# Performance work log

Measured on AMD Instinct MI355X. Metric: run time of the kernel, lower is better.

The kernel has to match this reference:

```python
import jax, jax.numpy as jnp
import numpy as np
import math

ENC_MAX = 64
DEC_MAX = 128


def _tran_mask(M):
    # faithful reconstruction of self.tran and self.mask buffers
    fs = math.log(DEC_MAX / (DEC_MAX + ENC_MAX))  # fixed_shift_p
    fe = math.log(ENC_MAX / (DEC_MAX + ENC_MAX))  # fixed_emit_p
    i = np.arange(M)[:, None]
    j = np.arange(M)[None, :]
    tran = np.where(i + j < M, (M - (i + j) - 1) * fs + fe, 0.0).astype(np.float32)
    # mask_br: -inf where i+j >= M (anti-diagonal i+j==M-1 stays 0)
    mask = np.where(i + j >= M, -np.inf, 0.0).astype(np.float32)
    return jnp.asarray(tran), jnp.asarray(mask)


def _lstm(xs, Wih, Whh, bih, bhh):
    # xs: [L, in]; torch LSTM gate order i,f,g,o; batch=1 handled as unbatched
    H = Whh.shape[1]
    def step(carry, xt):
        h, c = carry
        g = Wih @ xt + bih + Whh @ h + bhh  # [4H]
        i, f, gg, o = jnp.split(g, 4)
        c = jax.nn.sigmoid(f) * c + jax.nn.sigmoid(i) * jnp.tanh(gg)
        h = jax.nn.sigmoid(o) * jnp.tanh(c)
        return (h, c), h
    _, hs = jax.lax.scan(step, (jnp.zeros((H,), xs.dtype), jnp.zeros((H,), xs.dtype)), xs)
    return hs  # [L, H]


def setup_inputs() -> dict:
    key = jax.random.key(0)
    ks = jax.random.split(key, 16)
    V, E, H, K, T = 32000, 100, 512, ENC_MAX, DEC_MAX
    def p(k, shape, scale):
        return jax.random.normal(k, shape, dtype=jnp.float32) * scale
    return {
        "x": jax.random.randint(ks[0], (1, K), 0, V),
        "y": jax.random.randint(ks[1], (1, T), 0, V),
        "emb": p(ks[2], (V, E), 0.1),
        "enc_Wih": p(ks[3], (4 * H, E), 1.0 / np.sqrt(E)),
        "enc_Whh": p(ks[4], (4 * H, H), 1.0 / np.sqrt(H)),
        "enc_bih": jnp.zeros((4 * H,), jnp.float32),
        "enc_bhh": jnp.zeros((4 * H,), jnp.float32),
        "dec_Wih": p(ks[5], (4 * H, E), 1.0 / np.sqrt(E)),
        "dec_Whh": p(ks[6], (4 * H, H), 1.0 / np.sqrt(H)),
        "dec_bih": jnp.zeros((4 * H,), jnp.float32),
        "dec_bhh": jnp.zeros((4 * H,), jnp.float32),
        "Weh": p(ks[7], (E, 2 * H), 1.0 / np.sqrt(2 * H)),  # emit_hidden
        "beh": jnp.zeros((E,), jnp.float32),
        "Wem": p(ks[8], (V, E), 1.0 / np.sqrt(E)),  # emit
        "bem": jnp.zeros((V,), jnp.float32),
    }


def reference(x, y, emb, enc_Wih, enc_Whh, enc_bih, enc_bhh,
              dec_Wih, dec_Whh, dec_bih, dec_bhh, Weh, beh, Wem, bem):
    K = x.shape[1]
    T = y.shape[1]
    x_emb = emb[x[0]]            # [K, E]
    y_emb = emb[y[0]]            # [T, E]
    Eenc = _lstm(x_emb, enc_Wih, enc_Whh, enc_bih, enc_bhh)  # [K, H]
    D = _lstm(y_emb, dec_Wih, dec_Whh, dec_bih, dec_bhh)     # [T, H]

    tran, mask = _tran_mask(ENC_MAX)
    tranm = tran[ENC_MAX - K:, :K] + mask[ENC_MAX - K:, :K]  # [K, K]

    # emissions for all steps at once (joint = cat(E, D_{t-1}) -> relu -> emit -> log_softmax -> gather word_t)
    H = Eenc.shape[1]
    We_E, We_D = Weh[:, :H], Weh[:, H:]
    hpre = jax.nn.relu(Eenc @ We_E.T + (D[:T - 1] @ We_D.T)[:, None, :] + beh)  # [T-1, K, E]
    logits = jnp.einsum('tke,ve->tkv', hpre, Wem) + bem                          # [T-1, K, V]
    words = y[0, 1:]                                                             # [T-1]
    gathered = jnp.take_along_axis(logits, words[:, None, None], axis=2)[..., 0]  # [T-1, K]
    emission = gathered - jax.scipy.special.logsumexp(logits, axis=2)             # [T-1, K]

    def step(pre_alpha, em_t):
        scores = pre_alpha[:, None] + tranm            # [K(i), K(j)]
        mx = jnp.max(scores, axis=0)                   # [K]
        ind = jnp.argmax(scores, axis=0).astype(jnp.int32)
        mx = jnp.flip(mx)                              # self.flip
        ind = jnp.flip(ind)
        new = mx + em_t
        return new, ind

    pre_alpha, inds = jax.lax.scan(step, jnp.zeros((K,), jnp.float32), emission)
    indices = jnp.concatenate([jnp.zeros((1, K), jnp.int32), inds], axis=0)  # [T, K]

    val = pre_alpha[K - 1]  # align_last

    def bstep(ind, idx_row):
        nind = idx_row[ind]
        return nind, nind
    _, alignments = jax.lax.scan(bstep, jnp.int32(K - 1), indices, reverse=True)  # [T]
    return alignments, val
```

## Files before the change

### kernel.cpp

```cpp
#include <hip/hip_runtime.h>


#define K_ENC 64
#define HID   512
#define EMB   100
#define VOC   32000
#define G4    2048

typedef __attribute__((ext_vector_type(8))) short  short8;
typedef __attribute__((ext_vector_type(4))) float  f32x4;
typedef __attribute__((ext_vector_type(4))) int    i32x4;
typedef unsigned long long u64;

#define LOG2E 1.4426950408889634f
#define LN2   0.6931471805599453f

__device__ __forceinline__ unsigned short f2bf(float f) {
  union { float f; unsigned u; } x; x.f = f;
  unsigned r = x.u + 0x7FFFu + ((x.u >> 16) & 1u);
  return (unsigned short)(r >> 16);
}

__device__ __forceinline__ float fast_sigmoid(float x) {
  return __builtin_amdgcn_rcpf(1.f + __builtin_amdgcn_exp2f(-LOG2E * x));
}
__device__ __forceinline__ float fast_tanh(float x) {
  return 1.f - 2.f * __builtin_amdgcn_rcpf(1.f + __builtin_amdgcn_exp2f(2.f * LOG2E * x));
}

#define OFF_PAD   0
#define OFF_HBUF  256
#define OFF_G0E   4352
#define OFF_G0D   135424
#define OFF_EENC  395520
#define OFF_D     428288
#define OFF_EWE   493312
#define OFF_DWD   499712
#define OFF_BEM   512412
#define OFF_SUM   544412
#define OFF_EM    552540
#define OFF_WEM   560668

__global__ void kZero(float* __restrict__ ws) {
  int gid = blockIdx.x * 256 + threadIdx.x;
  if (gid < 4352) ws[gid] = 0.f;
  else if (gid < 4352 + 127 * 64) ws[OFF_SUM + gid - 4352] = 0.f;
}

__global__ __launch_bounds__(256) void kG0(const int* __restrict__ x, const int* __restrict__ y,
                    const float* __restrict__ emb,
                    const float* __restrict__ eWih, const float* __restrict__ ebih,
                    const float* __restrict__ ebhh,
                    const float* __restrict__ dWih, const float* __restrict__ dbih,
                    const float* __restrict__ dbhh,
                    float* __restrict__ ws) {
  int gid = blockIdx.x * 256 + threadIdx.x;
  const int enc_total = K_ENC * G4;
  if (gid >= enc_total + 127 * G4) return;
  bool enc = gid < enc_total;
  int loc = enc ? gid : gid - enc_total;
  int t = loc >> 11, r = loc & (G4 - 1);
  int tok = enc ? x[t] : y[t];
  const float* Wr = (enc ? eWih : dWih) + r * EMB;
  const float* er = emb + tok * EMB;
  float s = 0.f;
  #pragma unroll 4
  for (int e = 0; e < EMB; ++e) s += er[e] * Wr[e];
  s += enc ? (ebih[r] + ebhh[r]) : (dbih[r] + dbhh[r]);
  ws[(enc ? OFF_G0E : OFF_G0D) + t * G4 + r] = s;
}

__global__ __launch_bounds__(256) void kWemPrep(const float* __restrict__ Wem,
                                               const float* __restrict__ bem,
                                               float* __restrict__ ws) {
  int gid = blockIdx.x * 256 + threadIdx.x;
  int vt = gid >> 11;
  int kb = (gid >> 9) & 3;
  int L  = (gid >> 3) & 63;
  int j  = gid & 7;
  int v = vt * 16 + (L & 15);
  int k = kb * 32 + ((L >> 4) << 3) + j;
  float val = (k < EMB) ? Wem[v * EMB + k] : 0.f;
  ((unsigned short*)(ws + OFF_WEM))[gid] = f2bf(val);
  if (gid < VOC) ws[OFF_BEM + gid] = bem[gid] * LOG2E;
}

#define STEP_GUARD 16384

__global__ __launch_bounds__(512, 2) void kLstm(const float* __restrict__ eWhh,
                                                const float* __restrict__ dWhh,
                                                float* __restrict__ ws) {
  const int grp = blockIdx.x >> 5;
  const int wg  = blockIdx.x & 31;
  const float* __restrict__ Whh = grp ? dWhh : eWhh;
  const float* __restrict__ G0  = ws + (grp ? OFF_G0D : OFF_G0E);
  float* hs = ws + (grp ? OFF_D : OFF_EENC);
  u64* hb = (u64*)(ws + OFF_HBUF) + grp * 1024;
  const int steps = grp ? 127 : K_ENC;
  const int tid = threadIdx.x;
  const int jl = tid >> 5, sub = tid & 31;
  const int j = wg * 16 + jl;
  __shared__ float h_lds[32 * 20];

  float cst = 0.f;
  for (int t = 0; t < steps; ++t) {
    float4 w4[16];
    #pragma unroll
    for (int g = 0; g < 4; ++g)
      #pragma unroll
      for (int q = 0; q < 4; ++q)
        w4[g * 4 + q] = *(const float4*)&Whh[(g * HID + j) * HID + sub * 16 + q * 4];
    float g0i = G0[t * G4 + j];
    float g0f = G0[t * G4 + HID + j];
    float g0g = G0[t * G4 + 2 * HID + j];
    float g0o = G0[t * G4 + 3 * HID + j];
    if (tid < 256) {
      const u64* src = hb + (t & 1) * 512 + tid * 2;
      i32x4 v;
      int guard = 0;
      for (;;) {
        asm volatile("global_load_dwordx4 %0, %1, off sc0 sc1\n\t"
                     "s_waitcnt vmcnt(0)"
                     : "=v"(v) : "v"(src) : "memory");
        if ((v[1] == t && v[3] == t) || ++guard >= STEP_GUARD) break;
        __builtin_amdgcn_s_sleep(1);
      }
      int k0 = tid * 2, k1 = k0 + 1;
      union { int u; float f; } c0, c1; c0.u = v[0]; c1.u = v[2];
      h_lds[(k0 >> 4) * 20 + (k0 & 15)] = c0.f;
      h_lds[(k1 >> 4) * 20 + (k1 & 15)] = c1.f;
    }
    __syncthreads();
    float h[16];
    #pragma unroll
    for (int kk = 0; kk < 16; ++kk) h[kk] = h_lds[sub * 20 + kk];
    float p0 = 0.f, p1 = 0.f, p2 = 0.f, p3 = 0.f;
    #pragma unroll
    for (int q = 0; q < 4; ++q) {
      p0 += w4[0+q].x*h[q*4+0] + w4[0+q].y*h[q*4+1] + w4[0+q].z*h[q*4+2] + w4[0+q].w*h[q*4+3];
      p1 += w4[4+q].x*h[q*4+0] + w4[4+q].y*h[q*4+1] + w4[4+q].z*h[q*4+2] + w4[4+q].w*h[q*4+3];
      p2 += w4[8+q].x*h[q*4+0] + w4[8+q].y*h[q*4+1] + w4[8+q].z*h[q*4+2] + w4[8+q].w*h[q*4+3];
      p3 += w4[12+q].x*h[q*4+0] + w4[12+q].y*h[q*4+1] + w4[12+q].z*h[q*4+2] + w4[12+q].w*h[q*4+3];
    }
    #pragma unroll
    for (int d = 1; d <= 16; d <<= 1) {
      p0 += __shfl_xor(p0, d); p1 += __shfl_xor(p1, d);
      p2 += __shfl_xor(p2, d); p3 += __shfl_xor(p3, d);
    }
    float si = fast_sigmoid(g0i + p0);
    float sf = fast_sigmoid(g0f + p1);
    float gG = fast_tanh(g0g + p2);
    float so = fast_sigmoid(g0o + p3);
    cst = sf * cst + si * gG;
    float hn = so * fast_tanh(cst);
    if (sub == 0) {
      union { float f; unsigned u; } hu; hu.f = hn;
      u64 pack = ((u64)(unsigned)(t + 1) << 32) | (u64)hu.u;
      atomicExch(&hb[((t + 1) & 1) * 512 + j], pack);
      hs[t * HID + j] = hn;
    }
    __syncthreads();
  }
}

__global__ __launch_bounds__(256) void kProj(const float* __restrict__ Weh,
                                             const float* __restrict__ beh,
                                             float* __restrict__ ws) {
  int bid = blockIdx.x;
  bool enc = bid < K_ENC;
  int row = enc ? bid : bid - K_ENC;
  const float* in = ws + (enc ? OFF_EENC : OFF_D) + row * HID;
  __shared__ float sin_[HID];
  int tid = threadIdx.x;
  sin_[tid] = in[tid]; sin_[tid + 256] = in[tid + 256];
  __syncthreads();
  if (tid < EMB) {
    const float* wr = Weh + tid * 1024 + (enc ? 0 : HID);
    float s = 0.f;
    #pragma unroll 4
    for (int h = 0; h < HID; ++h) s += sin_[h] * wr[h];
    if (!enc) s += beh[tid];
    ws[(enc ? OFF_EWE : OFF_DWD) + row * EMB + tid] = s * LOG2E;
  }
}

__global__ __launch_bounds__(256) void kLogits(float* __restrict__ ws) {
  const int t = blockIdx.x >> 2;
  const int chunk = blockIdx.x & 3;
  const int tid = threadIdx.x;
  const int lane = tid & 63;
  const int wv = tid >> 6;
  const int quad = lane >> 4, l15 = lane & 15;
  __shared__ __align__(16) unsigned short A[64 * 128];
  const float* EWe = ws + OFF_EWE;
  const float* DWd = ws + OFF_DWD + t * EMB;
  for (int idx = tid; idx < 64 * 128; idx += 256) {
    int m = idx >> 7, k = idx & 127;
    float hv = 0.f;
    if (k < EMB) { float s = EWe[m * EMB + k] + DWd[k]; hv = s > 0.f ? s : 0.f; }
    A[idx] = f2bf(hv);
  }
  __syncthreads();
  short8 af[4][4];
  #pragma unroll
  for (int mt = 0; mt < 4; ++mt)
    #pragma unroll
    for (int kb = 0; kb < 4; ++kb)
      af[mt][kb] = *(const short8*)&A[(mt * 16 + l15) * 128 + kb * 32 + quad * 8];
  const unsigned short* wem = (const unsigned short*)(ws + OFF_WEM);
  const float* bem_s = ws + OFF_BEM;
  float rs[4][4];
  #pragma unroll
  for (int a = 0; a < 4; ++a)
    #pragma unroll
    for (int b = 0; b < 4; ++b) rs[a][b] = 0.f;
  int vt = chunk * 500 + wv;
  short8 nb0, nb1, nb2, nb3; float nbi;
  nb0 = *(const short8*)&wem[(vt * 4 + 0) * 512 + lane * 8];
  nb1 = *(const short8*)&wem[(vt * 4 + 1) * 512 + lane * 8];
  nb2 = *(const short8*)&wem[(vt * 4 + 2) * 512 + lane * 8];
  nb3 = *(const short8*)&wem[(vt * 4 + 3) * 512 + lane * 8];
  nbi = bem_s[vt * 16 + l15];
  for (int ii = wv; ii < 500; ii += 4) {
    short8 cb0 = nb0, cb1 = nb1, cb2 = nb2, cb3 = nb3;
    float cbi = nbi;
    int nvt = vt + 4;
    if (ii + 4 < 500) {
      nb0 = *(const short8*)&wem[(nvt * 4 + 0) * 512 + lane * 8];
      nb1 = *(const short8*)&wem[(nvt * 4 + 1) * 512 + lane * 8];
      nb2 = *(const short8*)&wem[(nvt * 4 + 2) * 512 + lane * 8];
      nb3 = *(const short8*)&wem[(nvt * 4 + 3) * 512 + lane * 8];
      nbi = bem_s[nvt * 16 + l15];
    }
    f32x4 acc[4];
    #pragma unroll
    for (int mt = 0; mt < 4; ++mt) acc[mt] = (f32x4){cbi, cbi, cbi, cbi};
    #pragma unroll
    for (int mt = 0; mt < 4; ++mt) {
      acc[mt] = __builtin_amdgcn_mfma_f32_16x16x32_bf16(af[mt][0], cb0, acc[mt], 0, 0, 0);
      acc[mt] = __builtin_amdgcn_mfma_f32_16x16x32_bf16(af[mt][1], cb1, acc[mt], 0, 0, 0);
      acc[mt] = __builtin_amdgcn_mfma_f32_16x16x32_bf16(af[mt][2], cb2, acc[mt], 0, 0, 0);
      acc[mt] = __builtin_amdgcn_mfma_f32_16x16x32_bf16(af[mt][3], cb3, acc[mt], 0, 0, 0);
    }
    #pragma unroll
    for (int mt = 0; mt < 4; ++mt)
      #pragma unroll
      for (int r = 0; r < 4; ++r)
        rs[mt][r] += __builtin_amdgcn_exp2f(acc[mt][r]);
    vt = nvt;
  }
  #pragma unroll
  for (int d = 1; d < 16; d <<= 1)
    #pragma unroll
    for (int mt = 0; mt < 4; ++mt)
      #pragma unroll
      for (int r = 0; r < 4; ++r)
        rs[mt][r] += __shfl_xor(rs[mt][r], d);
  if (l15 == 0) {
    float* sum = ws + OFF_SUM + t * 64;
    #pragma unroll
    for (int mt = 0; mt < 4; ++mt)
      #pragma unroll
      for (int r = 0; r < 4; ++r)
        atomicAdd(&sum[mt * 16 + quad * 4 + r], rs[mt][r]);
  }
}

__global__ __launch_bounds__(256) void kEmission(const int* __restrict__ y,
                                                 const float* __restrict__ Wem,
                                                 float* __restrict__ ws) {
  int gid = blockIdx.x * 256 + threadIdx.x;
  if (gid >= 127 * 64) return;
  int t = gid >> 6, m = gid & 63;
  const float* ew = ws + OFF_EWE + m * EMB;
  const float* dw = ws + OFF_DWD + t * EMB;
  int wt = y[t + 1];
  const float* wr = Wem + wt * EMB;
  float s = ws[OFF_BEM + wt];
  #pragma unroll 4
  for (int e = 0; e < EMB; ++e) {
    float h = ew[e] + dw[e];
    h = h > 0.f ? h : 0.f;
    s += h * wr[e];
  }
  ws[OFF_EM + gid] = LN2 * (s - __builtin_amdgcn_logf(ws[OFF_SUM + gid]));
}

__global__ __launch_bounds__(256) void kViterbi(const float* __restrict__ ws, float* __restrict__ out) {
  __shared__ float em_lds[127 * 64];
  __shared__ int   inds[128 * 64];
  __shared__ float sval;
  const int tid = threadIdx.x;
  for (int i = tid; i < 127 * 64; i += 256) em_lds[i] = ws[OFF_EM + i];
  if (tid < 64) inds[tid] = 0;
  __syncthreads();
  if (tid < 64) {
    const int j = tid;
    const float fs = -0.4054651081081644f;
    const float fe = -1.0986122886681098f;
    float pa = 0.f;
    float emnext = em_lds[j];
    for (int t = 0; t < 127; ++t) {
      float emc = emnext;
      if (t < 126) emnext = em_lds[(t + 1) * 64 + j];
      float v = fmaf(-fs, (float)j, pa);
      int idx = j;
      #pragma unroll
      for (int d = 1; d < 64; d <<= 1) {
        float vv = __shfl_up(v, d);
        int   ii = __shfl_up(idx, d);
        bool cur = v > vv;
        v   = cur ? v : vv;
        idx = cur ? idx : ii;
      }
      pa = v + fe + fs * (float)j + emc;
      inds[(t + 1) * 64 + j] = idx;
    }
    if (j == 63) sval = pa;
  }
  __syncthreads();
  if (tid == 0) {
    int ind = 63;
    for (int t = 127; t >= 0; --t) {
      ind = inds[t * 64 + ind];
      out[t] = (float)ind;
    }
    out[128] = sval;
  }
}

extern "C" void kernel_launch(void* const* d_in, const int* in_sizes, int n_in,
                              void* d_out, int out_size, void* d_ws, size_t ws_size,
                              hipStream_t stream) {
  const int*   x    = (const int*)d_in[0];
  const int*   y    = (const int*)d_in[1];
  const float* emb  = (const float*)d_in[2];
  const float* eWih = (const float*)d_in[3];
  const float* eWhh = (const float*)d_in[4];
  const float* ebih = (const float*)d_in[5];
  const float* ebhh = (const float*)d_in[6];
  const float* dWih = (const float*)d_in[7];
  const float* dWhh = (const float*)d_in[8];
  const float* dbih = (const float*)d_in[9];
  const float* dbhh = (const float*)d_in[10];
  const float* Weh  = (const float*)d_in[11];
  const float* beh  = (const float*)d_in[12];
  const float* Wem  = (const float*)d_in[13];
  const float* bem  = (const float*)d_in[14];
  float* ws  = (float*)d_ws;
  float* out = (float*)d_out;

  hipLaunchKernelGGL(kZero,     dim3(49),    dim3(256), 0, stream, ws);
  hipLaunchKernelGGL(kG0,       dim3(1528),  dim3(256), 0, stream, x, y, emb, eWih, ebih, ebhh, dWih, dbih, dbhh, ws);
  hipLaunchKernelGGL(kWemPrep,  dim3(16000), dim3(256), 0, stream, Wem, bem, ws);
  hipLaunchKernelGGL(kLstm,     dim3(64),    dim3(512), 0, stream, eWhh, dWhh, ws);
  hipLaunchKernelGGL(kProj,     dim3(191),   dim3(256), 0, stream, Weh, beh, ws);
  hipLaunchKernelGGL(kLogits,   dim3(508),   dim3(256), 0, stream, ws);
  hipLaunchKernelGGL(kEmission, dim3(32),    dim3(256), 0, stream, y, Wem, ws);
  hipLaunchKernelGGL(kViterbi,  dim3(1),     dim3(256), 0, stream, ws, out);
}
```

Before: 510.3 us.

## Fuse prep kernels, double-buffer LSTM LDS, and tile logits over four timesteps

Merges the zero, G0 and Wem-prep kernels into one launch to cut launch overhead. In the LSTM, the hidden-state LDS buffer is double-buffered so one of the two block barriers per step can go, and the sleep in the spin-wait is removed. The logits kernel now processes four timesteps per block with swizzled LDS, so each Wem tile loaded from global memory is reused four times. Partial sums are reduced in LDS before the global atomics. This costs more LDS and registers per block, and re-reads A fragments from LDS instead of holding them in registers.

```diff
diff --git a/kernel.cpp b/kernel.cpp
--- a/kernel.cpp
+++ b/kernel.cpp
@@ -41,48 +41,49 @@
 #define OFF_EM    552540
 #define OFF_WEM   560668
 
-__global__ void kZero(float* __restrict__ ws) {
-  int gid = blockIdx.x * 256 + threadIdx.x;
-  if (gid < 4352) ws[gid] = 0.f;
-  else if (gid < 4352 + 127 * 64) ws[OFF_SUM + gid - 4352] = 0.f;
-}
-
-__global__ __launch_bounds__(256) void kG0(const int* __restrict__ x, const int* __restrict__ y,
+#define PREP_WEM_BLKS 16000
+#define PREP_G0_BLKS  1528
+__global__ __launch_bounds__(256) void kPrep(const int* __restrict__ x, const int* __restrict__ y,
                     const float* __restrict__ emb,
                     const float* __restrict__ eWih, const float* __restrict__ ebih,
                     const float* __restrict__ ebhh,
                     const float* __restrict__ dWih, const float* __restrict__ dbih,
                     const float* __restrict__ dbhh,
+                    const float* __restrict__ Wem, const float* __restrict__ bem,
                     float* __restrict__ ws) {
-  int gid = blockIdx.x * 256 + threadIdx.x;
-  const int enc_total = K_ENC * G4;
-  if (gid >= enc_total + 127 * G4) return;
-  bool enc = gid < enc_total;
-  int loc = enc ? gid : gid - enc_total;
-  int t = loc >> 11, r = loc & (G4 - 1);
-  int tok = enc ? x[t] : y[t];
-  const float* Wr = (enc ? eWih : dWih) + r * EMB;
-  const float* er = emb + tok * EMB;
-  float s = 0.f;
-  #pragma unroll 4
-  for (int e = 0; e < EMB; ++e) s += er[e] * Wr[e];
-  s += enc ? (ebih[r] + ebhh[r]) : (dbih[r] + dbhh[r]);
-  ws[(enc ? OFF_G0E : OFF_G0D) + t * G4 + r] = s;
-}
-
-__global__ __launch_bounds__(256) void kWemPrep(const float* __restrict__ Wem,
-                                               const float* __restrict__ bem,
-                                               float* __restrict__ ws) {
-  int gid = blockIdx.x * 256 + threadIdx.x;
-  int vt = gid >> 11;
-  int kb = (gid >> 9) & 3;
-  int L  = (gid >> 3) & 63;
-  int j  = gid & 7;
-  int v = vt * 16 + (L & 15);
-  int k = kb * 32 + ((L >> 4) << 3) + j;
-  float val = (k < EMB) ? Wem[v * EMB + k] : 0.f;
-  ((unsigned short*)(ws + OFF_WEM))[gid] = f2bf(val);
-  if (gid < VOC) ws[OFF_BEM + gid] = bem[gid] * LOG2E;
+  const int b = blockIdx.x;
+  const int tid = threadIdx.x;
+  if (b < PREP_WEM_BLKS) {
+    int gid = b * 256 + tid;
+    int vt = gid >> 11;
+    int kb = (gid >> 9) & 3;
+    int L  = (gid >> 3) & 63;
+    int j  = gid & 7;
+    int v = vt * 16 + (L & 15);
+    int k = kb * 32 + ((L >> 4) << 3) + j;
+    float val = (k < EMB) ? Wem[v * EMB + k] : 0.f;
+    ((unsigned short*)(ws + OFF_WEM))[gid] = f2bf(val);
+    if (gid < VOC) ws[OFF_BEM + gid] = bem[gid] * LOG2E;
+  } else if (b < PREP_WEM_BLKS + PREP_G0_BLKS) {
+    int gid = (b - PREP_WEM_BLKS) * 256 + tid;
+    const int enc_total = K_ENC * G4;
+    if (gid >= enc_total + 127 * G4) return;
+    bool enc = gid < enc_total;
+    int loc = enc ? gid : gid - enc_total;
+    int t = loc >> 11, r = loc & (G4 - 1);
+    int tok = enc ? x[t] : y[t];
+    const float* Wr = (enc ? eWih : dWih) + r * EMB;
+    const float* er = emb + tok * EMB;
+    float s = 0.f;
+    #pragma unroll 4
+    for (int e = 0; e < EMB; ++e) s += er[e] * Wr[e];
+    s += enc ? (ebih[r] + ebhh[r]) : (dbih[r] + dbhh[r]);
+    ws[(enc ? OFF_G0E : OFF_G0D) + t * G4 + r] = s;
+  } else {
+    int gid = (b - PREP_WEM_BLKS - PREP_G0_BLKS) * 256 + tid;
+    if (gid < 4352) ws[gid] = 0.f;
+    else if (gid < 4352 + 127 * 64) ws[OFF_SUM + gid - 4352] = 0.f;
+  }
 }
 
 #define STEP_GUARD 16384
@@ -100,7 +101,7 @@
   const int tid = threadIdx.x;
   const int jl = tid >> 5, sub = tid & 31;
   const int j = wg * 16 + jl;
-  __shared__ float h_lds[32 * 20];
+  __shared__ float h_lds[2][32 * 20];
 
   float cst = 0.f;
   for (int t = 0; t < steps; ++t) {
@@ -123,17 +124,16 @@
                      "s_waitcnt vmcnt(0)"
                      : "=v"(v) : "v"(src) : "memory");
         if ((v[1] == t && v[3] == t) || ++guard >= STEP_GUARD) break;
-        __builtin_amdgcn_s_sleep(1);
       }
       int k0 = tid * 2, k1 = k0 + 1;
       union { int u; float f; } c0, c1; c0.u = v[0]; c1.u = v[2];
-      h_lds[(k0 >> 4) * 20 + (k0 & 15)] = c0.f;
-      h_lds[(k1 >> 4) * 20 + (k1 & 15)] = c1.f;
+      h_lds[t & 1][(k0 >> 4) * 20 + (k0 & 15)] = c0.f;
+      h_lds[t & 1][(k1 >> 4) * 20 + (k1 & 15)] = c1.f;
     }
     __syncthreads();
     float h[16];
     #pragma unroll
-    for (int kk = 0; kk < 16; ++kk) h[kk] = h_lds[sub * 20 + kk];
+    for (int kk = 0; kk < 16; ++kk) h[kk] = h_lds[t & 1][sub * 20 + kk];
     float p0 = 0.f, p1 = 0.f, p2 = 0.f, p3 = 0.f;
     #pragma unroll
     for (int q = 0; q < 4; ++q) {
@@ -159,7 +159,6 @@
       atomicExch(&hb[((t + 1) & 1) * 512 + j], pack);
       hs[t * HID + j] = hn;
     }
-    __syncthreads();
   }
 }
 
@@ -185,84 +184,100 @@
 }
 
 __global__ __launch_bounds__(256) void kLogits(float* __restrict__ ws) {
-  const int t = blockIdx.x >> 2;
-  const int chunk = blockIdx.x & 3;
+  const int tg = blockIdx.x >> 4;
+  const int chunk = blockIdx.x & 15;
   const int tid = threadIdx.x;
   const int lane = tid & 63;
   const int wv = tid >> 6;
   const int quad = lane >> 4, l15 = lane & 15;
-  __shared__ __align__(16) unsigned short A[64 * 128];
+  __shared__ __align__(16) unsigned short A[4][64 * 128];
+  __shared__ float psum[4][64];
+  if (tid < 256) { psum[tid >> 6][tid & 63] = 0.f; }
   const float* EWe = ws + OFF_EWE;
-  const float* DWd = ws + OFF_DWD + t * EMB;
   for (int idx = tid; idx < 64 * 128; idx += 256) {
     int m = idx >> 7, k = idx & 127;
-    float hv = 0.f;
-    if (k < EMB) { float s = EWe[m * EMB + k] + DWd[k]; hv = s > 0.f ? s : 0.f; }
-    A[idx] = f2bf(hv);
-  }
-  __syncthreads();
-  short8 af[4][4];
-  #pragma unroll
-  for (int mt = 0; mt < 4; ++mt)
-    #pragma unroll
-    for (int kb = 0; kb < 4; ++kb)
-      af[mt][kb] = *(const short8*)&A[(mt * 16 + l15) * 128 + kb * 32 + quad * 8];
+    bool kv = k < EMB;
+    float e = kv ? EWe[m * EMB + k] : 0.f;
+    int kswz = ((((k >> 3) ^ (m & 7)) << 3) | (k & 7));
+    #pragma unroll
+    for (int ts = 0; ts < 4; ++ts) {
+      int t = tg * 4 + ts; if (t > 126) t = 126;
+      float hv = 0.f;
+      if (kv) { float s = e + ws[OFF_DWD + t * EMB + k]; hv = s > 0.f ? s : 0.f; }
+      A[ts][(m << 7) | kswz] = f2bf(hv);
+    }
+  }
+  __syncthreads();
   const unsigned short* wem = (const unsigned short*)(ws + OFF_WEM);
   const float* bem_s = ws + OFF_BEM;
-  float rs[4][4];
+  float rs[4][4][4];
   #pragma unroll
   for (int a = 0; a < 4; ++a)
     #pragma unroll
-    for (int b = 0; b < 4; ++b) rs[a][b] = 0.f;
-  int vt = chunk * 500 + wv;
-  short8 nb0, nb1, nb2, nb3; float nbi;
-  nb0 = *(const short8*)&wem[(vt * 4 + 0) * 512 + lane * 8];
-  nb1 = *(const short8*)&wem[(vt * 4 + 1) * 512 + lane * 8];
-  nb2 = *(const short8*)&wem[(vt * 4 + 2) * 512 + lane * 8];
-  nb3 = *(const short8*)&wem[(vt * 4 + 3) * 512 + lane * 8];
+    for (int b = 0; b < 4; ++b)
+      #pragma unroll
+      for (int c = 0; c < 4; ++c) rs[a][b][c] = 0.f;
+  int vt = chunk * 125 + wv;
+  short8 nb[4]; float nbi;
+  #pragma unroll
+  for (int kb = 0; kb < 4; ++kb)
+    nb[kb] = *(const short8*)&wem[(vt * 4 + kb) * 512 + lane * 8];
   nbi = bem_s[vt * 16 + l15];
-  for (int ii = wv; ii < 500; ii += 4) {
-    short8 cb0 = nb0, cb1 = nb1, cb2 = nb2, cb3 = nb3;
-    float cbi = nbi;
+  for (int ii = wv; ii < 125; ii += 4) {
+    short8 cb[4]; float cbi = nbi;
+    #pragma unroll
+    for (int kb = 0; kb < 4; ++kb) cb[kb] = nb[kb];
     int nvt = vt + 4;
-    if (ii + 4 < 500) {
-      nb0 = *(const short8*)&wem[(nvt * 4 + 0) * 512 + lane * 8];
-      nb1 = *(const short8*)&wem[(nvt * 4 + 1) * 512 + lane * 8];
-      nb2 = *(const short8*)&wem[(nvt * 4 + 2) * 512 + lane * 8];
-      nb3 = *(const short8*)&wem[(nvt * 4 + 3) * 512 + lane * 8];
+    if (ii + 4 < 125) {
+      #pragma unroll
+      for (int kb = 0; kb < 4; ++kb)
+        nb[kb] = *(const short8*)&wem[(nvt * 4 + kb) * 512 + lane * 8];
       nbi = bem_s[nvt * 16 + l15];
     }
-    f32x4 acc[4];
-    #pragma unroll
-    for (int mt = 0; mt < 4; ++mt) acc[mt] = (f32x4){cbi, cbi, cbi, cbi};
-    #pragma unroll
-    for (int mt = 0; mt < 4; ++mt) {
-      acc[mt] = __builtin_amdgcn_mfma_f32_16x16x32_bf16(af[mt][0], cb0, acc[mt], 0, 0, 0);
-      acc[mt] = __builtin_amdgcn_mfma_f32_16x16x32_bf16(af[mt][1], cb1, acc[mt], 0, 0, 0);
-      acc[mt] = __builtin_amdgcn_mfma_f32_16x16x32_bf16(af[mt][2], cb2, acc[mt], 0, 0, 0);
-      acc[mt] = __builtin_amdgcn_mfma_f32_16x16x32_bf16(af[mt][3], cb3, acc[mt], 0, 0, 0);
-    }
-    #pragma unroll
-    for (int mt = 0; mt < 4; ++mt)
-      #pragma unroll
-      for (int r = 0; r < 4; ++r)
-        rs[mt][r] += __builtin_amdgcn_exp2f(acc[mt][r]);
+    #pragma unroll
+    for (int ts = 0; ts < 4; ++ts) {
+      f32x4 acc[4];
+      #pragma unroll
+      for (int mt = 0; mt < 4; ++mt) acc[mt] = (f32x4){cbi, cbi, cbi, cbi};
+      #pragma unroll
+      for (int mt = 0; mt < 4; ++mt)
+        #pragma unroll
+        for (int kb = 0; kb < 4; ++kb) {
+          short8 af = *(const short8*)&A[ts][((mt * 16 + l15) << 7) |
+                                            ((((kb * 4 + quad) ^ (l15 & 7))) << 3)];
+          acc[mt] = __builtin_amdgcn_mfma_f32_16x16x32_bf16(af, cb[kb], acc[mt], 0, 0, 0);
+        }
+      #pragma unroll
+      for (int mt = 0; mt < 4; ++mt)
+        #pragma unroll
+        for (int r = 0; r < 4; ++r)
+          rs[ts][mt][r] += __builtin_amdgcn_exp2f(acc[mt][r]);
+    }
     vt = nvt;
   }
   #pragma unroll
   for (int d = 1; d < 16; d <<= 1)
     #pragma unroll
-    for (int mt = 0; mt < 4; ++mt)
-      #pragma unroll
-      for (int r = 0; r < 4; ++r)
-        rs[mt][r] += __shfl_xor(rs[mt][r], d);
+    for (int ts = 0; ts < 4; ++ts)
+      #pragma unroll
+      for (int mt = 0; mt < 4; ++mt)
+        #pragma unroll
+        for (int r = 0; r < 4; ++r)
+          rs[ts][mt][r] += __shfl_xor(rs[ts][mt][r], d);
   if (l15 == 0) {
-    float* sum = ws + OFF_SUM + t * 64;
-    #pragma unroll
-    for (int mt = 0; mt < 4; ++mt)
-      #pragma unroll
-      for (int r = 0; r < 4; ++r)
-        atomicAdd(&sum[mt * 16 + quad * 4 + r], rs[mt][r]);
+    #pragma unroll
+    for (int ts = 0; ts < 4; ++ts)
+      #pragma unroll
+      for (int mt = 0; mt < 4; ++mt)
+        #pragma unroll
+        for (int r = 0; r < 4; ++r)
+          atomicAdd(&psum[ts][mt * 16 + quad * 4 + r], rs[ts][mt][r]);
+  }
+  __syncthreads();
+  if (tid < 256) {
+    int ts = tid >> 6, c = tid & 63;
+    int t = tg * 4 + ts;
+    if (t <= 126) atomicAdd(&ws[OFF_SUM + t * 64 + c], psum[ts][c]);
   }
 }
 
@@ -350,12 +365,11 @@
   float* ws  = (float*)d_ws;
   float* out = (float*)d_out;
 
-  hipLaunchKernelGGL(kZero,     dim3(49),    dim3(256), 0, stream, ws);
-  hipLaunchKernelGGL(kG0,       dim3(1528),  dim3(256), 0, stream, x, y, emb, eWih, ebih, ebhh, dWih, dbih, dbhh, ws);
-  hipLaunchKernelGGL(kWemPrep,  dim3(16000), dim3(256), 0, stream, Wem, bem, ws);
+  hipLaunchKernelGGL(kPrep,     dim3(PREP_WEM_BLKS + PREP_G0_BLKS + 49), dim3(256), 0, stream,
+                     x, y, emb, eWih, ebih, ebhh, dWih, dbih, dbhh, Wem, bem, ws);
   hipLaunchKernelGGL(kLstm,     dim3(64),    dim3(512), 0, stream, eWhh, dWhh, ws);
   hipLaunchKernelGGL(kProj,     dim3(191),   dim3(256), 0, stream, Weh, beh, ws);
-  hipLaunchKernelGGL(kLogits,   dim3(508),   dim3(256), 0, stream, ws);
+  hipLaunchKernelGGL(kLogits,   dim3(512),   dim3(256), 0, stream, ws);
   hipLaunchKernelGGL(kEmission, dim3(32),    dim3(256), 0, stream, y, Wem, ws);
   hipLaunchKernelGGL(kViterbi,  dim3(1),     dim3(256), 0, stream, ws, out);
 }
```

Result: slower. 644.1 us (+26.2%).
